# Optimization experiments

Measured on AMD Instinct MI355X. Metric: run time of the kernel, lower is better.

## Reference

```python
import jax, jax.numpy as jnp
import numpy as np

B, S, IK, IV = 16, 2048, 3, 1
D = IK + IV          # input_size = 4
H = 256              # hidden_size
F = 512              # dim_feedforward
L = 2                # num_layers
EPS = 1e-5


def setup_inputs() -> dict:
    key = jax.random.key(0)
    ks = jax.random.split(key, 16)
    n = jax.random.normal
    inp = {
        'KEY': n(ks[0], (B, S, IK), jnp.float32),
        'VALUE': n(ks[1], (B, S, IV), jnp.float32),
        # per-layer kernel-attention projections (stacked on layer axis)
        'Wq': n(ks[2], (L, D, H), jnp.float32) * 0.1,
        'bq': jnp.zeros((L, H), jnp.float32),
        'Wk': n(ks[3], (L, D, H), jnp.float32) * 0.1,
        'bk': jnp.zeros((L, H), jnp.float32),
        'Wv': n(ks[4], (L, D, H), jnp.float32) * 0.1,
        'bv': jnp.zeros((L, H), jnp.float32),
        'Wo': n(ks[5], (L, H, D), jnp.float32) * 0.1,
        'bo': jnp.zeros((L, D), jnp.float32),
        'bw': jnp.ones((L,), jnp.float32),          # Gaussian kernel bandwidth
        # LayerNorm 1
        'g1': jnp.ones((L, D), jnp.float32),
        'be1': jnp.zeros((L, D), jnp.float32),
        # FFN
        'W1': n(ks[6], (L, D, F), jnp.float32) * 0.1,
        'b1': jnp.zeros((L, F), jnp.float32),
        'W2': n(ks[7], (L, F, D), jnp.float32) * 0.1,
        'b2': jnp.zeros((L, D), jnp.float32),
        # LayerNorm 2
        'g2': jnp.ones((L, D), jnp.float32),
        'be2': jnp.zeros((L, D), jnp.float32),
        # final fc: input_size -> input_v
        'Wfc': n(ks[8], (D, IV), jnp.float32) * 0.1,
        'bfc': jnp.zeros((IV,), jnp.float32),
    }
    return inp


def _layernorm(x, g, b):
    m = x.mean(-1, keepdims=True)
    v = ((x - m) ** 2).mean(-1, keepdims=True)
    return (x - m) * jax.lax.rsqrt(v + EPS) * g + b


def reference(KEY, VALUE, Wq, bq, Wk, bk, Wv, bv, Wo, bo, bw,
              g1, be1, W1, b1, W2, b2, g2, be2, Wfc, bfc):
    # positioning: concat coords and values -> [B, S, D]
    X = jnp.concatenate([KEY, VALUE], axis=-1)
    n_layers = Wq.shape[0]
    for i in range(n_layers):
        # Nadaraya-Watson Gaussian kernel attention (madsnn, type='nwd', kernel='gauss')
        Q = X @ Wq[i] + bq[i]                      # [B,S,H]
        K = X @ Wk[i] + bk[i]                      # [B,S,H]
        V = X @ Wv[i] + bv[i]                      # [B,S,H]
        # pairwise squared distances ||q-k||^2, [B,S,S]
        d2 = ((Q * Q).sum(-1)[:, :, None]
              + (K * K).sum(-1)[:, None, :]
              - 2.0 * jnp.einsum('bqh,bkh->bqk', Q, K))
        attn = jax.nn.softmax(-0.5 * d2 * (bw[i] ** 2), axis=-1)
        attn_out = jnp.einsum('bqk,bkh->bqh', attn, V) @ Wo[i] + bo[i]  # [B,S,D]
        # residual + LayerNorm + FFN + residual + LayerNorm (dropout = identity in eval)
        res = _layernorm(X + attn_out, g1[i], be1[i])
        ff = jax.nn.relu(res @ W1[i] + b1[i]) @ W2[i] + b2[i]
        X = _layernorm(res + ff, g2[i], be2[i])
    return X @ Wfc + bfc                            # [B,S,IV]
```

## Files before the change

kernel.cpp:

```cpp
#include <hip/hip_runtime.h>

#define BB 16
#define SS 2048
#define NTOK (BB*SS)
#define NPAIR (NTOK/2)
#define PLANE (NPAIR*4)
#define FF 512
#define EPSF 1e-5f
#define QW 16

#if __has_builtin(__builtin_amdgcn_exp2f)
#define EXP2F(x) __builtin_amdgcn_exp2f(x)
#else
#define EXP2F(x) exp2f(x)
#endif

typedef float v2f __attribute__((ext_vector_type(2)));


__device__ __forceinline__ float wred64(float v) {
#pragma unroll
  for (int m = 32; m > 0; m >>= 1) v += __shfl_xor(v, m, 64);
  return v;
}

__device__ __forceinline__ float rflf(float v) {
  union { float f; int i; } u; u.f = v;
  u.i = __builtin_amdgcn_readfirstlane(u.i);
  return u.f;
}


__global__ __launch_bounds__(64) void prep_kernel(
    const float* __restrict__ Wq, const float* __restrict__ bq,
    const float* __restrict__ Wk, const float* __restrict__ bk,
    const float* __restrict__ Wv, const float* __restrict__ bv,
    const float* __restrict__ Wo, const float* __restrict__ bw,
    const float* __restrict__ W1, const float* __restrict__ b1,
    const float* __restrict__ W2,
    float* __restrict__ sm, float* __restrict__ w1t)
{
  const int i = blockIdx.x;
  const int lane = threadIdx.x;
  float m4[4][4] = {{0}}, gkk[4][4] = {{0}}, wvo[4][4] = {{0}};
  float akk[4] = {0}, bvo[4] = {0};
  float ck1 = 0.f, ck2 = 0.f;

  for (int h = lane; h < 256; h += 64) {
    float vq[4], vk[4], vv[4], wo4[4];
#pragma unroll
    for (int a = 0; a < 4; ++a) {
      vq[a]  = Wq[(i*4 + a)*256 + h];
      vk[a]  = Wk[(i*4 + a)*256 + h];
      vv[a]  = Wv[(i*4 + a)*256 + h];
      wo4[a] = Wo[(i*256 + h)*4 + a];
    }
    const float bqh = bq[i*256 + h], bkh = bk[i*256 + h], bvh = bv[i*256 + h];
#pragma unroll
    for (int a = 0; a < 4; ++a) {
#pragma unroll
      for (int c = 0; c < 4; ++c) {
        m4[a][c]  = fmaf(vq[a], vk[c], m4[a][c]);
        gkk[a][c] = fmaf(vk[a], vk[c], gkk[a][c]);
        wvo[a][c] = fmaf(vv[a], wo4[c], wvo[a][c]);
      }
      akk[a] = fmaf(vk[a], bqh - bkh, akk[a]);
      bvo[a] = fmaf(bvh, wo4[a], bvo[a]);
    }
    ck1 = fmaf(bqh, bkh, ck1);
    ck2 = fmaf(bkh, bkh, ck2);
  }
#pragma unroll
  for (int a = 0; a < 4; ++a) {
#pragma unroll
    for (int c = 0; c < 4; ++c) {
      m4[a][c]  = wred64(m4[a][c]);
      gkk[a][c] = wred64(gkk[a][c]);
      wvo[a][c] = wred64(wvo[a][c]);
    }
    akk[a] = wred64(akk[a]);
    bvo[a] = wred64(bvo[a]);
  }
  ck1 = wred64(ck1); ck2 = wred64(ck2);

  if (lane == 0) {
    const float bwv = bw[i];
    const float bw2 = bwv * bwv * 1.44269504088896f;
    float* s = sm + i*64;
#pragma unroll
    for (int a = 0; a < 4; ++a) {
#pragma unroll
      for (int c = 0; c < 4; ++c) {
        s[a*4+c]      = bw2 * m4[a][c];
        s[16 + a*4+c] = -0.5f * bw2 * gkk[a][c];
        s[32 + a*4+c] = wvo[a][c];
      }
      s[48+a] = bw2 * akk[a];
      s[52+a] = bvo[a];
    }
    s[56] = bw2 * (ck1 - 0.5f * ck2);
  }
  for (int f = lane; f < FF; f += 64) {
    float* rec = w1t + (i*FF + f)*12;
#pragma unroll
    for (int c = 0; c < 4; ++c) rec[c]   = W1[(i*4 + c)*FF + f];
#pragma unroll
    for (int c = 0; c < 4; ++c) rec[4+c] = W2[(i*FF + f)*4 + c];
    rec[8] = b1[i*FF + f];
    rec[9] = 0.f; rec[10] = 0.f; rec[11] = 0.f;
  }
}

__device__ __forceinline__ void compute_feat(const float x[4], const float* __restrict__ s,
                                             float* __restrict__ featrec)
{
  float P[4], VT[4], tk[4];
#pragma unroll
  for (int a = 0; a < 4; ++a) {
    P[a]  = fmaf(s[a*4+3], x[3], fmaf(s[a*4+2], x[2], fmaf(s[a*4+1], x[1], s[a*4+0]*x[0])));
    tk[a] = fmaf(s[16+a*4+3], x[3], fmaf(s[16+a*4+2], x[2], fmaf(s[16+a*4+1], x[1], s[16+a*4+0]*x[0])));
    VT[a] = s[52+a] + fmaf(s[32+3*4+a], x[3], fmaf(s[32+2*4+a], x[2], fmaf(s[32+1*4+a], x[1], s[32+0*4+a]*x[0])));
  }
  float R = s[56];
#pragma unroll
  for (int a = 0; a < 4; ++a) R = fmaf(tk[a] + s[48+a], x[a], R);
  featrec[0]=P[0]; featrec[1]=P[1]; featrec[2]=P[2]; featrec[3]=P[3];
  featrec[4]=VT[0]; featrec[5]=VT[1]; featrec[6]=VT[2]; featrec[7]=VT[3];
  featrec[8]=R;
}

__global__ __launch_bounds__(256) void feat_kernel(
    const float* __restrict__ KEY, const float* __restrict__ VALUE,
    const float* __restrict__ sm, float* __restrict__ feat)
{
  const int p = blockIdx.x*256 + threadIdx.x;
  const int ta = 2*p, tb = 2*p + 1;
  float xa[4] = {KEY[ta*3], KEY[ta*3+1], KEY[ta*3+2], VALUE[ta]};
  float xb[4] = {KEY[tb*3], KEY[tb*3+1], KEY[tb*3+2], VALUE[tb]};
  float fa[9], fb[9];
  compute_feat(xa, sm, fa);
  compute_feat(xb, sm, fb);
#pragma unroll
  for (int pl = 0; pl < 4; ++pl) {
    *(float4*)(feat + (size_t)pl*PLANE + (size_t)p*4) =
        make_float4(fa[2*pl], fb[2*pl], fa[2*pl+1], fb[2*pl+1]);
  }
  *(float4*)(feat + (size_t)4*PLANE + (size_t)p*4) =
      make_float4(fa[8], fb[8], 0.f, 0.f);
}

__device__ __forceinline__ void ln4(const float t[4], const float* __restrict__ g,
                                    const float* __restrict__ b, float r[4])
{
  const float m = 0.25f*(t[0]+t[1]+t[2]+t[3]);
  const float d0 = t[0]-m, d1 = t[1]-m, d2 = t[2]-m, d3 = t[3]-m;
  const float v = 0.25f*(d0*d0 + d1*d1 + d2*d2 + d3*d3);
  const float sc = rsqrtf(v + EPSF);
  r[0] = fmaf(d0*sc, g[0], b[0]);
  r[1] = fmaf(d1*sc, g[1], b[1]);
  r[2] = fmaf(d2*sc, g[2], b[2]);
  r[3] = fmaf(d3*sc, g[3], b[3]);
}

__global__ __launch_bounds__(256, 2) void layer_kernel(
    const float* __restrict__ KEY, const float* __restrict__ VALUE,
    const float* __restrict__ X, const float* __restrict__ feat,
    const float* __restrict__ w1t, const float* __restrict__ smn,
    const float* __restrict__ bo, const float* __restrict__ g1, const float* __restrict__ be1,
    const float* __restrict__ b2v, const float* __restrict__ g2, const float* __restrict__ be2,
    float* __restrict__ Xout, float* __restrict__ featout,
    const float* __restrict__ Wfc, const float* __restrict__ bfc,
    float* __restrict__ outp, int first, int last)
{
  const int bid = blockIdx.x;
  const int b = bid >> 5, qg = bid & 31;
  const int qbase = (b << 11) + (qg << 6);
  const int tid = threadIdx.x;
  const int lane = tid & 63, wv = tid >> 6;
  const int q0 = qbase + wv*QW;

  __shared__ float sums[4*QW*9];
  __shared__ float ress[64*4];
  __shared__ float redf[4*64*4];

  float qx0[QW], qx1[QW], qx2[QW], qx3[QW];
#pragma unroll
  for (int q = 0; q < QW; ++q) {
    const int gq = q0 + q;
    float a, b_, c, d;
    if (first) {
      a = KEY[gq*3]; b_ = KEY[gq*3+1]; c = KEY[gq*3+2]; d = VALUE[gq];
    } else {
      const float4 xv = *(const float4*)(X + (size_t)gq*4);
      a = xv.x; b_ = xv.y; c = xv.z; d = xv.w;
    }
    qx0[q] = rflf(a); qx1[q] = rflf(b_); qx2[q] = rflf(c); qx3[q] = rflf(d);
  }

  v2f aV0[QW], aV1[QW], aV2[QW], aV3[QW], aD[QW];
#pragma unroll
  for (int q = 0; q < QW; ++q) {
    aV0[q] = v2f{0.f,0.f}; aV1[q] = v2f{0.f,0.f};
    aV2[q] = v2f{0.f,0.f}; aV3[q] = v2f{0.f,0.f};
    aD[q]  = v2f{0.f,0.f};
  }

  const int pb = (b << 10) + lane;

  auto PROC = [&](const float4& A, const float4& Bf, const float4& C,
                  const float4& D, const float4& E) {
    const v2f P0 = v2f{A.x, A.y},   P1 = v2f{A.z, A.w};
    const v2f P2 = v2f{Bf.x, Bf.y}, P3 = v2f{Bf.z, Bf.w};
    const v2f V0 = v2f{C.x, C.y},   V1 = v2f{C.z, C.w};
    const v2f V2 = v2f{D.x, D.y},   V3 = v2f{D.z, D.w};
    const v2f Rp = v2f{E.x, E.y};
#pragma unroll
    for (int q = 0; q < QW; ++q) {
      v2f l = __builtin_elementwise_fma(P0, v2f{qx0[q], qx0[q]}, Rp);
      l = __builtin_elementwise_fma(P1, v2f{qx1[q], qx1[q]}, l);
      l = __builtin_elementwise_fma(P2, v2f{qx2[q], qx2[q]}, l);
      l = __builtin_elementwise_fma(P3, v2f{qx3[q], qx3[q]}, l);
      const v2f e = v2f{EXP2F(l.x), EXP2F(l.y)};
      aV0[q] = __builtin_elementwise_fma(e, V0, aV0[q]);
      aV1[q] = __builtin_elementwise_fma(e, V1, aV1[q]);
      aV2[q] = __builtin_elementwise_fma(e, V2, aV2[q]);
      aV3[q] = __builtin_elementwise_fma(e, V3, aV3[q]);
      aD[q] += e;
    }
  };

#define LDCH(A_, B_, C_, D_, E_, it_) {                                  \
    const size_t o = (size_t)(pb + ((it_) << 6)) * 4;                    \
    A_ = *(const float4*)(feat + o);                                     \
    B_ = *(const float4*)(feat + (size_t)PLANE + o);                     \
    C_ = *(const float4*)(feat + (size_t)2*PLANE + o);                   \
    D_ = *(const float4*)(feat + (size_t)3*PLANE + o);                   \
    E_ = *(const float4*)(feat + (size_t)4*PLANE + o); }

  float4 pA, pB, pC, pD, pE;
  float4 nA, nB, nC, nD, nE;
  LDCH(pA, pB, pC, pD, pE, 0);
#pragma unroll
  for (int it = 0; it < 16; it += 2) {
    LDCH(nA, nB, nC, nD, nE, it + 1);
    PROC(pA, pB, pC, pD, pE);
    if (it + 2 < 16) LDCH(pA, pB, pC, pD, pE, it + 2);
    PROC(nA, nB, nC, nD, nE);
  }
#undef LDCH

  float s[QW][5];
#pragma unroll
  for (int q = 0; q < QW; ++q) {
    s[q][0] = aV0[q].x + aV0[q].y;
    s[q][1] = aV1[q].x + aV1[q].y;
    s[q][2] = aV2[q].x + aV2[q].y;
    s[q][3] = aV3[q].x + aV3[q].y;
    s[q][4] = aD[q].x + aD[q].y;
  }
#pragma unroll
  for (int q = 0; q < QW; ++q)
#pragma unroll
    for (int c = 0; c < 5; ++c) s[q][c] = wred64(s[q][c]);

  if (lane == 0) {
    float* dst = sums + wv*(QW*9);
#pragma unroll
    for (int q = 0; q < QW; ++q) {
#pragma unroll
      for (int c = 0; c < 5; ++c) dst[q*9 + c] = s[q][c];
    }
  }
  __syncthreads();

  if (tid < 64) {
    const float* sv = sums + tid*9;
    const float inv = 1.0f / sv[4];
    const int gq = qbase + tid;
    float xv0, xv1, xv2, xv3;
    if (first) {
      xv0 = KEY[gq*3]; xv1 = KEY[gq*3+1]; xv2 = KEY[gq*3+2]; xv3 = VALUE[gq];
    } else {
      const float4 xv = *(const float4*)(X + (size_t)gq*4);
      xv0 = xv.x; xv1 = xv.y; xv2 = xv.z; xv3 = xv.w;
    }
    float t4[4];
    t4[0] = xv0 + fmaf(sv[0], inv, bo[0]);
    t4[1] = xv1 + fmaf(sv[1], inv, bo[1]);
    t4[2] = xv2 + fmaf(sv[2], inv, bo[2]);
    t4[3] = xv3 + fmaf(sv[3], inv, bo[3]);
    float r[4];
    ln4(t4, g1, be1, r);
    *(float4*)(ress + tid*4) = make_float4(r[0], r[1], r[2], r[3]);
  }
  __syncthreads();

  const int tok = lane, fc = wv;
  const float4 rv = *(const float4*)(ress + tok*4);
  float fa0 = 0.f, fa1 = 0.f, fa2 = 0.f, fa3 = 0.f;
  const float* wt = w1t + (size_t)fc*128*12;
#pragma unroll 4
  for (int f = 0; f < 128; ++f) {
    const float* rec = wt + f*12;
    const float4 w1r = *(const float4*)rec;
    const float4 w2r = *(const float4*)(rec + 4);
    const float b1f = rec[8];
    float h = fmaf(rv.w, w1r.w, fmaf(rv.z, w1r.z, fmaf(rv.y, w1r.y, fmaf(rv.x, w1r.x, b1f))));
    h = fmaxf(h, 0.f);
    fa0 = fmaf(h, w2r.x, fa0);
    fa1 = fmaf(h, w2r.y, fa1);
    fa2 = fmaf(h, w2r.z, fa2);
    fa3 = fmaf(h, w2r.w, fa3);
  }
  *(float4*)(redf + (size_t)((fc << 6) + tok)*4) = make_float4(fa0, fa1, fa2, fa3);
  __syncthreads();

  if (tid < 64) {
    float t2[4];
#pragma unroll
    for (int c = 0; c < 4; ++c) {
      float sa = b2v[c];
#pragma unroll
      for (int k = 0; k < 4; ++k) sa += redf[(size_t)((k << 6) + tid)*4 + c];
      t2[c] = ress[tid*4 + c] + sa;
    }
    float y[4];
    ln4(t2, g2, be2, y);
    const int gq = qbase + tid;
    if (last) {
      outp[gq] = fmaf(y[3], Wfc[3], fmaf(y[2], Wfc[2], fmaf(y[1], Wfc[1], fmaf(y[0], Wfc[0], bfc[0]))));
    } else {
      *(float4*)(Xout + (size_t)gq*4) = make_float4(y[0], y[1], y[2], y[3]);
      float fr[9];
      compute_feat(y, smn, fr);
      const int p = gq >> 1, par = gq & 1;
#pragma unroll
      for (int c = 0; c < 8; ++c)
        featout[(size_t)(c >> 1)*PLANE + (size_t)p*4 + (c & 1)*2 + par] = fr[c];
      featout[(size_t)4*PLANE + (size_t)p*4 + par] = fr[8];
    }
  }
}

extern "C" void kernel_launch(void* const* d_in, const int* in_sizes, int n_in,
                              void* d_out, int out_size, void* d_ws, size_t ws_size,
                              hipStream_t stream)
{
  const float* KEY   = (const float*)d_in[0];
  const float* VALUE = (const float*)d_in[1];
  const float* Wq  = (const float*)d_in[2];
  const float* bq  = (const float*)d_in[3];
  const float* Wk  = (const float*)d_in[4];
  const float* bk  = (const float*)d_in[5];
  const float* Wv  = (const float*)d_in[6];
  const float* bv  = (const float*)d_in[7];
  const float* Wo  = (const float*)d_in[8];
  const float* bo  = (const float*)d_in[9];
  const float* bw  = (const float*)d_in[10];
  const float* g1  = (const float*)d_in[11];
  const float* be1 = (const float*)d_in[12];
  const float* W1  = (const float*)d_in[13];
  const float* b1  = (const float*)d_in[14];
  const float* W2  = (const float*)d_in[15];
  const float* b2  = (const float*)d_in[16];
  const float* g2  = (const float*)d_in[17];
  const float* be2 = (const float*)d_in[18];
  const float* Wfc = (const float*)d_in[19];
  const float* bfc = (const float*)d_in[20];
  float* out = (float*)d_out;

  float* w    = (float*)d_ws;
  float* sm   = w;
  float* w1t  = w + 128;
  float* X1   = w + 12416;
  float* f0   = w + 143488;
  float* f1   = w + 471168;

  prep_kernel<<<2, 64, 0, stream>>>(Wq, bq, Wk, bk, Wv, bv, Wo, bw,
                                    W1, b1, W2, sm, w1t);
  feat_kernel<<<64, 256, 0, stream>>>(KEY, VALUE, sm, f0);

  layer_kernel<<<512, 256, 0, stream>>>(KEY, VALUE, X1, f0,
      w1t, sm + 64,
      bo, g1, be1, b2, g2, be2,
      X1, f1, Wfc, bfc, out, 1, 0);

  layer_kernel<<<512, 256, 0, stream>>>(KEY, VALUE, X1, f1,
      w1t + FF*12, sm,
      bo + 4, g1 + 4, be1 + 4, b2 + 4, g2 + 4, be2 + 4,
      X1, f1, Wfc, bfc, out, 0, 1);
}
```

Before: 189.2 us.

## Halve queries per wave to double grid and raise occupancy in layer kernel

Each wave now handles 8 query tokens instead of 16, so each block covers 32 queries and the grid doubles to 1024 blocks, with launch bounds raised to 4 blocks per SM. The manual double-buffered feature-load pipeline is replaced by a simple unrolled loop that leaves load scheduling to the compiler. The FFN stage is re-split across 8 groups of 32 tokens to match. The intent is less register pressure and more resident waves to hide memory latency. The cost is that every key chunk is re-read twice as often per query and the explicit prefetch is lost.

```diff
diff --git a/kernel.cpp b/kernel.cpp
--- a/kernel.cpp
+++ b/kernel.cpp
@@ -7,7 +7,7 @@
 #define PLANE (NPAIR*4)
 #define FF 512
 #define EPSF 1e-5f
-#define QW 16
+#define QW 8
 
 #if __has_builtin(__builtin_amdgcn_exp2f)
 #define EXP2F(x) __builtin_amdgcn_exp2f(x)
@@ -162,7 +162,7 @@
   r[3] = fmaf(d3*sc, g[3], b[3]);
 }
 
-__global__ __launch_bounds__(256, 2) void layer_kernel(
+__global__ __launch_bounds__(256, 4) void layer_kernel(
     const float* __restrict__ KEY, const float* __restrict__ VALUE,
     const float* __restrict__ X, const float* __restrict__ feat,
     const float* __restrict__ w1t, const float* __restrict__ smn,
@@ -173,15 +173,15 @@
     float* __restrict__ outp, int first, int last)
 {
   const int bid = blockIdx.x;
-  const int b = bid >> 5, qg = bid & 31;
-  const int qbase = (b << 11) + (qg << 6);
+  const int b = bid >> 6, qg = bid & 63;
+  const int qbase = (b << 11) + (qg << 5);
   const int tid = threadIdx.x;
   const int lane = tid & 63, wv = tid >> 6;
   const int q0 = qbase + wv*QW;
 
   __shared__ float sums[4*QW*9];
-  __shared__ float ress[64*4];
-  __shared__ float redf[4*64*4];
+  __shared__ float ress[32*4];
+  __shared__ float redf[8*32*4];
 
   float qx0[QW], qx1[QW], qx2[QW], qx3[QW];
 #pragma unroll
@@ -206,9 +206,14 @@
   }
 
   const int pb = (b << 10) + lane;
-
-  auto PROC = [&](const float4& A, const float4& Bf, const float4& C,
-                  const float4& D, const float4& E) {
+#pragma unroll 4
+  for (int it = 0; it < 16; ++it) {
+    const size_t o = (size_t)(pb + (it << 6)) * 4;
+    const float4 A  = *(const float4*)(feat + o);
+    const float4 Bf = *(const float4*)(feat + (size_t)PLANE + o);
+    const float4 C  = *(const float4*)(feat + (size_t)2*PLANE + o);
+    const float4 D  = *(const float4*)(feat + (size_t)3*PLANE + o);
+    const float4 E  = *(const float4*)(feat + (size_t)4*PLANE + o);
     const v2f P0 = v2f{A.x, A.y},   P1 = v2f{A.z, A.w};
     const v2f P2 = v2f{Bf.x, Bf.y}, P3 = v2f{Bf.z, Bf.w};
     const v2f V0 = v2f{C.x, C.y},   V1 = v2f{C.z, C.w};
@@ -227,27 +232,7 @@
       aV3[q] = __builtin_elementwise_fma(e, V3, aV3[q]);
       aD[q] += e;
     }
-  };
-
-#define LDCH(A_, B_, C_, D_, E_, it_) {                                  \
-    const size_t o = (size_t)(pb + ((it_) << 6)) * 4;                    \
-    A_ = *(const float4*)(feat + o);                                     \
-    B_ = *(const float4*)(feat + (size_t)PLANE + o);                     \
-    C_ = *(const float4*)(feat + (size_t)2*PLANE + o);                   \
-    D_ = *(const float4*)(feat + (size_t)3*PLANE + o);                   \
-    E_ = *(const float4*)(feat + (size_t)4*PLANE + o); }
-
-  float4 pA, pB, pC, pD, pE;
-  float4 nA, nB, nC, nD, nE;
-  LDCH(pA, pB, pC, pD, pE, 0);
-#pragma unroll
-  for (int it = 0; it < 16; it += 2) {
-    LDCH(nA, nB, nC, nD, nE, it + 1);
-    PROC(pA, pB, pC, pD, pE);
-    if (it + 2 < 16) LDCH(pA, pB, pC, pD, pE, it + 2);
-    PROC(nA, nB, nC, nD, nE);
-  }
-#undef LDCH
+  }
 
   float s[QW][5];
 #pragma unroll
@@ -273,7 +258,7 @@
   }
   __syncthreads();
 
-  if (tid < 64) {
+  if (tid < 32) {
     const float* sv = sums + tid*9;
     const float inv = 1.0f / sv[4];
     const int gq = qbase + tid;
@@ -295,12 +280,12 @@
   }
   __syncthreads();
 
-  const int tok = lane, fc = wv;
+  const int tok = tid & 31, fc = tid >> 5;
   const float4 rv = *(const float4*)(ress + tok*4);
   float fa0 = 0.f, fa1 = 0.f, fa2 = 0.f, fa3 = 0.f;
-  const float* wt = w1t + (size_t)fc*128*12;
+  const float* wt = w1t + (size_t)fc*64*12;
 #pragma unroll 4
-  for (int f = 0; f < 128; ++f) {
+  for (int f = 0; f < 64; ++f) {
     const float* rec = wt + f*12;
     const float4 w1r = *(const float4*)rec;
     const float4 w2r = *(const float4*)(rec + 4);
@@ -312,16 +297,16 @@
     fa2 = fmaf(h, w2r.z, fa2);
     fa3 = fmaf(h, w2r.w, fa3);
   }
-  *(float4*)(redf + (size_t)((fc << 6) + tok)*4) = make_float4(fa0, fa1, fa2, fa3);
+  *(float4*)(redf + (size_t)((fc << 5) + tok)*4) = make_float4(fa0, fa1, fa2, fa3);
   __syncthreads();
 
-  if (tid < 64) {
+  if (tid < 32) {
     float t2[4];
 #pragma unroll
     for (int c = 0; c < 4; ++c) {
       float sa = b2v[c];
 #pragma unroll
-      for (int k = 0; k < 4; ++k) sa += redf[(size_t)((k << 6) + tid)*4 + c];
+      for (int k = 0; k < 8; ++k) sa += redf[(size_t)((k << 5) + tid)*4 + c];
       t2[c] = ress[tid*4 + c] + sa;
     }
     float y[4];
@@ -380,12 +365,12 @@
                                     W1, b1, W2, sm, w1t);
   feat_kernel<<<64, 256, 0, stream>>>(KEY, VALUE, sm, f0);
 
-  layer_kernel<<<512, 256, 0, stream>>>(KEY, VALUE, X1, f0,
+  layer_kernel<<<1024, 256, 0, stream>>>(KEY, VALUE, X1, f0,
       w1t, sm + 64,
       bo, g1, be1, b2, g2, be2,
       X1, f1, Wfc, bfc, out, 1, 0);
 
-  layer_kernel<<<512, 256, 0, stream>>>(KEY, VALUE, X1, f1,
+  layer_kernel<<<1024, 256, 0, stream>>>(KEY, VALUE, X1, f1,
       w1t + FF*12, sm,
       bo + 4, g1 + 4, be1 + 4, b2 + 4, g2 + 4, be2 + 4,
       X1, f1, Wfc, bfc, out, 0, 1);
```

Measured after the change: 187.2 us. Within noise of the previous version (-1.1%).
